# Kernel optimization log

Hardware: AMD Instinct MI355X
Metric: run time of the kernel (lower is better)

The kernel has to match this reference:

```python
import jax, jax.numpy as jnp
import numpy as np

V = 267735
D_PROJ = 1024
CUTOFF_ENDS = [0, 20000, 40000, 200000, V]   # cutoffs + [vocab]
DIV_VAL = 4
SEQ, BATCH = 64, 8


def setup_inputs() -> dict:
    key = jax.random.key(0)
    ks = jax.random.split(key, 20)
    s = 0.02
    inp = {}
    inp["hidden"] = jax.random.normal(ks[0], (SEQ, BATCH, D_PROJ), dtype=jnp.float32)
    inp["target"] = jax.random.randint(ks[1], (SEQ, BATCH), 0, V)
    n_clusters = len(CUTOFF_ENDS) - 2  # 3
    inp["cluster_weight"] = jax.random.normal(ks[2], (n_clusters, 1024), dtype=jnp.float32) * s
    inp["cluster_bias"] = jnp.zeros((n_clusters,), dtype=jnp.float32)
    k = 3
    for i in range(4):
        l, r = CUTOFF_ENDS[i], CUTOFF_ENDS[i + 1]
        d_i = 1024 // (DIV_VAL ** i)        # 1024, 256, 64, 16
        inp[f"W{i}"] = jax.random.normal(ks[k], (r - l, d_i), dtype=jnp.float32) * s; k += 1
        inp[f"b{i}"] = jnp.zeros((r - l,), dtype=jnp.float32)
        inp[f"proj{i}"] = jax.random.normal(ks[k], (d_i, D_PROJ), dtype=jnp.float32) * s; k += 1
    return inp


def _logit(x, W, b, proj):
    # x: [i,b,d_proj], proj: [d_emb_i, d_proj], W: [n, d_emb_i]
    y = jnp.einsum('ibd,ed->ibe', x, proj)
    return jnp.einsum('ibe,ne->ibn', y, W) + b


def reference(hidden, target, cluster_weight, cluster_bias,
              W0, b0, proj0, W1, b1, proj1, W2, b2, proj2, W3, b3, proj3):
    c0 = CUTOFF_ENDS[1]  # shortlist size (20000)
    # head: shortlist weights concatenated with cluster logits
    head_W = jnp.concatenate([W0, cluster_weight], axis=0)   # [c0 + n_clusters, 1024]
    head_b = jnp.concatenate([b0, cluster_bias], axis=0)
    head_logprob = jax.nn.log_softmax(_logit(hidden, head_W, head_b, proj0), axis=-1)
    out = [head_logprob[..., :c0]]
    tails = [(W1, b1, proj1), (W2, b2, proj2), (W3, b3, proj3)]
    for i, (W, b, proj) in enumerate(tails, start=1):
        tail_logprob = jax.nn.log_softmax(_logit(hidden, W, b, proj), axis=-1)
        # joint logprob = log P(cluster i) + log P(word | cluster i)
        out.append(head_logprob[..., c0 + i - 1, None] + tail_logprob)
    out = jnp.concatenate(out, axis=-1)  # [seq, batch, vocab] of log-probs
    # scatter/gather loss combine is equivalent to gathering the gold log-prob
    gold_lp = jnp.take_along_axis(out, target[..., None], axis=-1)[..., 0]
    loss = -jnp.mean(gold_lp)
    return out, loss
```

## Files before the change

### kernel.cpp

```cpp
#include <hip/hip_runtime.h>

typedef __attribute__((ext_vector_type(8))) short short8;
typedef __attribute__((ext_vector_type(4))) float f32x4;

#define LDC 267735L
#define OUT_ELEMS 137080320L
#define NB_TOT 2094
#define M_FIX 16.0f

__device__ __forceinline__ short f2bf(float f) {
    unsigned u = __float_as_uint(f);
    unsigned r = (u + 0x7fffu + ((u >> 16) & 1u)) >> 16;
    return (short)r;
}
__device__ __forceinline__ float bf2f(short s) {
    return __uint_as_float(((unsigned)(unsigned short)s) << 16);
}
__device__ __forceinline__ short8 cvt8v(f32x4 a, f32x4 b) {
    short8 r;
    r[0] = f2bf(a[0]); r[1] = f2bf(a[1]); r[2] = f2bf(a[2]); r[3] = f2bf(a[3]);
    r[4] = f2bf(b[0]); r[5] = f2bf(b[1]); r[6] = f2bf(b[2]); r[7] = f2bf(b[3]);
    return r;
}

__device__ __forceinline__ void gll16(const short* g, short* l) {
    __builtin_amdgcn_global_load_lds(
        (const __attribute__((address_space(1))) void*)g,
        (__attribute__((address_space(3))) void*)l, 16, 0, 0);
}

__device__ __forceinline__ void conv8(int e, const float* __restrict__ src,
                                      const float* __restrict__ ex, int Nsrc, int Nex,
                                      int Ksrc, int kshift, short* __restrict__ dst)
{
    int r = e >> kshift;
    int c = (e & ((1 << kshift) - 1)) << 3;
    const float* p = nullptr;
    if (r < Nsrc) p = src + (long)r * Ksrc + c;
    else if (r < Nsrc + Nex) p = ex + (long)(r - Nsrc) * Ksrc + c;
    short8 o = {0, 0, 0, 0, 0, 0, 0, 0};
    if (p != nullptr && c < Ksrc) {
        f32x4 a = *(const f32x4*)p;
        f32x4 b = *(const f32x4*)(p + 4);
        o = cvt8v(a, b);
    }
    *(short8*)(dst + (((long)r) << (kshift + 3)) + c) = o;
}

__global__ __launch_bounds__(256) void convert_all(
    const float* __restrict__ W0, const float* __restrict__ cw,
    const float* __restrict__ W1, const float* __restrict__ W2, const float* __restrict__ W3,
    const float* __restrict__ p0, const float* __restrict__ p1,
    const float* __restrict__ p2, const float* __restrict__ p3,
    const float* __restrict__ hidden,
    short* __restrict__ Wb0, short* __restrict__ Wb1,
    short* __restrict__ Wb2, short* __restrict__ Wb3,
    short* __restrict__ pb0, short* __restrict__ pb1,
    short* __restrict__ pb2, short* __restrict__ pb3,
    short* __restrict__ hb)
{
    int b = blockIdx.x;
    int tid = threadIdx.x;
    if (b < 10048)      { conv8((b          ) * 256 + tid, W0, cw, 20000, 3, 1024, 7, Wb0); }
    else if (b < 12560) { conv8((b - 10048  ) * 256 + tid, W1, nullptr, 20000, 0, 256, 5, Wb1); }
    else if (b < 17560) { conv8((b - 12560  ) * 256 + tid, W2, nullptr, 160000, 0, 64, 3, Wb2); }
    else if (b < 18620) { conv8((b - 17560  ) * 256 + tid, W3, nullptr, 67735, 0, 16, 2, Wb3); }
    else if (b < 19132) { conv8((b - 18620  ) * 256 + tid, p0, nullptr, 1024, 0, 1024, 7, pb0); }
    else if (b < 19260) { conv8((b - 19132  ) * 256 + tid, p1, nullptr, 256, 0, 1024, 7, pb1); }
    else if (b < 19324) { conv8((b - 19260  ) * 256 + tid, p2, nullptr, 64, 0, 1024, 7, pb2); }
    else if (b < 19388) { conv8((b - 19324  ) * 256 + tid, p3, nullptr, 16, 0, 1024, 7, pb3); }
    else                { conv8((b - 19388  ) * 256 + tid, hidden, nullptr, 512, 0, 1024, 7, hb); }
}

struct SegP {
    const short* A;
    const short* B;
    const float* bias;
    short* Cb;
    long ldcb;
    int lda, ldb, K, N, Nmain;
};
struct Seg4 { SegP s[4]; };

template<int MODE>
__global__ __launch_bounds__(256, 3) void gemm_uber(
    Seg4 segs, int e0, int e1, int e2,
    const float* __restrict__ cbias, float* __restrict__ clus,
    float* __restrict__ partMS)
{
    __shared__ short As[2][128 * 32];
    __shared__ short Bs[2][128 * 32];
    __shared__ float ps[2][128];

    int bx = blockIdx.x;
    int si = (bx < e0) ? 0 : (bx < e1) ? 1 : (bx < e2) ? 2 : 3;
    int sb = (si == 0) ? 0 : (si == 1) ? e0 : (si == 2) ? e1 : e2;
    const SegP sp = segs.s[si];

    int tid = threadIdx.x;
    int w = tid >> 6, l = tid & 63;
    int wm = w >> 1, wn = w & 1;
    int l15 = l & 15, g = l >> 4, k8 = g << 3;
    int rowBase = blockIdx.y << 7;
    int colBase = (bx - sb) << 7;

    int sr0 = (w << 5);
    int sr1 = sr0 + 16;
    int lrow = l >> 2;
    int kOff = (l & 3) << 3;
    const short* aG0 = sp.A + (long)(rowBase + sr0 + lrow) * sp.lda + kOff;
    const short* aG1 = sp.A + (long)(rowBase + sr1 + lrow) * sp.lda + kOff;
    const short* bG0 = sp.B + (long)(colBase + sr0 + lrow) * sp.ldb + kOff;
    const short* bG1 = sp.B + (long)(colBase + sr1 + lrow) * sp.ldb + kOff;
    int ldsA0 = sr0 << 5;
    int ldsA1 = sr1 << 5;

    f32x4 acc[4][4];
    #pragma unroll
    for (int i = 0; i < 4; ++i)
        #pragma unroll
        for (int j = 0; j < 4; ++j) acc[i][j] = f32x4{0.f, 0.f, 0.f, 0.f};

    int nt = sp.K >> 5;

    gll16(aG0, &As[0][ldsA0]);
    gll16(aG1, &As[0][ldsA1]);
    gll16(bG0, &Bs[0][ldsA0]);
    gll16(bG1, &Bs[0][ldsA1]);
    __syncthreads();

    int cur = 0;
    #pragma unroll 1
    for (int t = 0; t < nt; ++t) {
        int knext = (t + 1) << 5;
        if (t + 1 < nt) {
            int nb = cur ^ 1;
            gll16(aG0 + knext, &As[nb][ldsA0]);
            gll16(aG1 + knext, &As[nb][ldsA1]);
            gll16(bG0 + knext, &Bs[nb][ldsA0]);
            gll16(bG1 + knext, &Bs[nb][ldsA1]);
        }
        short8 af[4], bf[4];
        #pragma unroll
        for (int mi = 0; mi < 4; ++mi)
            af[mi] = *(const short8*)&As[cur][(((wm << 6) + (mi << 4) + l15) << 5) + k8];
        #pragma unroll
        for (int ni = 0; ni < 4; ++ni)
            bf[ni] = *(const short8*)&Bs[cur][(((wn << 6) + (ni << 4) + l15) << 5) + k8];
        #pragma unroll
        for (int mi = 0; mi < 4; ++mi)
            #pragma unroll
            for (int ni = 0; ni < 4; ++ni)
                acc[mi][ni] = __builtin_amdgcn_mfma_f32_16x16x32_bf16(
                    af[mi], bf[ni], acc[mi][ni], 0, 0, 0);
        __syncthreads();
        cur ^= 1;
    }

    int colv[4];
    float bv4[4];
    #pragma unroll
    for (int ni = 0; ni < 4; ++ni) {
        int col = colBase + (wn << 6) + (ni << 4) + l15;
        colv[ni] = col;
        float bval = 0.f;
        if (MODE == 1) {
            if (col < sp.Nmain) bval = sp.bias[col];
            else if (col < sp.N) bval = cbias[col - sp.Nmain];
        }
        bv4[ni] = bval;
    }

    #pragma unroll
    for (int mi = 0; mi < 4; ++mi) {
        #pragma unroll
        for (int r = 0; r < 4; ++r) {
            int srowg = rowBase + (wm << 6) + (mi << 4) + (g << 2) + r;
            float vals[4];
            #pragma unroll
            for (int ni = 0; ni < 4; ++ni) vals[ni] = acc[mi][ni][r] + bv4[ni];

            if (MODE == 0) {
                #pragma unroll
                for (int ni = 0; ni < 4; ++ni) {
                    int col = colv[ni];
                    if (col < (int)sp.ldcb)
                        sp.Cb[(long)srowg * sp.ldcb + col] = f2bf(vals[ni]);
                }
            } else {
                float s = 0.f;
                #pragma unroll
                for (int ni = 0; ni < 4; ++ni) {
                    int col = colv[ni];
                    if (col < sp.Nmain) {
                        sp.Cb[(long)srowg * sp.ldcb + col] = f2bf(vals[ni]);
                        s += __expf(vals[ni] - M_FIX);
                    } else if (col < sp.N) {
                        clus[srowg * 3 + (col - sp.Nmain)] = vals[ni];
                        s += __expf(vals[ni] - M_FIX);
                    }
                }
                #pragma unroll
                for (int d = 1; d < 16; d <<= 1) s += __shfl_xor(s, d);
                if (l15 == 0) {
                    int rl = (wm << 6) + (mi << 4) + (g << 2) + r;
                    ps[wn][rl] = s;
                }
            }
        }
    }
    if (MODE == 1) {
        __syncthreads();
        if (tid < 128) {
            float S = ps[0][tid] + ps[1][tid];
            partMS[(long)(rowBase + tid) * NB_TOT + bx] = S;
        }
    }
}

__global__ __launch_bounds__(256) void combine_adj(
    const float* __restrict__ partMS, const float* __restrict__ clus,
    float* __restrict__ adjA)
{
    const int segOff[4] = {0, 157, 314, 1564};
    const int segNb[4]  = {157, 157, 1250, 530};
    int row = blockIdx.x, tid = threadIdx.x;
    const float* p = partMS + (long)row * NB_TOT;
    __shared__ float ss[256], Ls[4];
    for (int seg = 0; seg < 4; ++seg) {
        float s = 0.f;
        for (int cb = segOff[seg] + tid; cb < segOff[seg] + segNb[seg]; cb += 256)
            s += p[cb];
        ss[tid] = s;
        __syncthreads();
        for (int off = 128; off > 0; off >>= 1) {
            if (tid < off) ss[tid] += ss[tid + off];
            __syncthreads();
        }
        if (tid == 0) Ls[seg] = logf(ss[0]) + M_FIX;
        __syncthreads();
    }
    if (tid == 0) {
        float l0 = Ls[0];
        adjA[row * 4 + 0] = -l0;
        adjA[row * 4 + 1] = clus[row * 3 + 0] - l0 - Ls[1];
        adjA[row * 4 + 2] = clus[row * 3 + 1] - l0 - Ls[2];
        adjA[row * 4 + 3] = clus[row * 3 + 2] - l0 - Ls[3];
    }
}

__global__ __launch_bounds__(256) void finalize2(
    const short* __restrict__ L0, const short* __restrict__ L1,
    const short* __restrict__ L2, const short* __restrict__ L3,
    const float* __restrict__ adjA, float* __restrict__ out)
{
    int row = blockIdx.y;
    long c0 = ((long)blockIdx.x * 256 + threadIdx.x) * 8;
    if (c0 >= 267735) return;
    const short* src; float adj; long off;
    if (c0 < 20000)       { src = L0 + (long)row * 20000;  off = c0;          adj = adjA[row*4+0]; }
    else if (c0 < 40000)  { src = L1 + (long)row * 20000;  off = c0 - 20000;  adj = adjA[row*4+1]; }
    else if (c0 < 200000) { src = L2 + (long)row * 160000; off = c0 - 40000;  adj = adjA[row*4+2]; }
    else                  { src = L3 + (long)row * 67736;  off = c0 - 200000; adj = adjA[row*4+3]; }
    float* po = out + (long)row * LDC + c0;
    if (c0 + 8 <= 267735) {
        short8 v = *(const short8*)(src + off);
        #pragma unroll
        for (int j = 0; j < 8; ++j) po[j] = bf2f(v[j]) + adj;
    } else {
        for (int j = 0; c0 + j < 267735; ++j) po[j] = bf2f(src[off + j]) + adj;
    }
}

__global__ __launch_bounds__(512) void loss_k(
    const float* __restrict__ out, const int* __restrict__ target,
    float* __restrict__ lossOut)
{
    int tid = threadIdx.x;
    int t = target[tid];
    float v = out[(long)tid * LDC + t];
    __shared__ float sbuf[512];
    sbuf[tid] = v;
    __syncthreads();
    for (int off = 256; off > 0; off >>= 1) {
        if (tid < off) sbuf[tid] += sbuf[tid + off];
        __syncthreads();
    }
    if (tid == 0) lossOut[0] = -sbuf[0] / 512.0f;
}

__device__ __forceinline__ short8 cvt8p(const float* p, bool valid) {
    short8 r = {0, 0, 0, 0, 0, 0, 0, 0};
    if (valid) {
        f32x4 a = *(const f32x4*)p;
        f32x4 b = *(const f32x4*)(p + 4);
        r = cvt8v(a, b);
    }
    return r;
}

#define LDT 40
__global__ __launch_bounds__(256, 2) void gemm_f32(
    const float* __restrict__ A, int lda,
    const float* __restrict__ B, int ldb,
    const float* __restrict__ Wex,
    const float* __restrict__ bias, const float* __restrict__ biasEx,
    float* __restrict__ C, long ldc, long colOffset,
    float* __restrict__ Cex,
    int N, int Nmain, int K)
{
    __shared__ short As[2][128 * LDT];
    __shared__ short Bs[2][128 * LDT];
    int tid = threadIdx.x;
    int w = tid >> 6, l = tid & 63;
    int wm = w >> 1, wn = w & 1;
    int l15 = l & 15, g = l >> 4, k8 = g << 3;
    int rowBase = blockIdx.y << 7;
    int colBase = blockIdx.x << 7;
    int srow = tid >> 1;
    int skc = (tid & 1) << 4;
    const float* aSrc = A + (long)(rowBase + srow) * lda + skc;
    int bn = colBase + srow;
    bool bnv = bn < N;
    const float* bRow = (Wex != nullptr && bn >= Nmain)
                          ? (Wex + (long)(bn - Nmain) * ldb)
                          : (B + (long)(bnv ? bn : 0) * ldb);
    const float* bSrc = bRow + skc;
    int ldsOff = srow * LDT + skc;
    f32x4 acc[4][4];
    #pragma unroll
    for (int i = 0; i < 4; ++i)
        #pragma unroll
        for (int j = 0; j < 4; ++j) acc[i][j] = f32x4{0.f, 0.f, 0.f, 0.f};
    int nt = (K + 31) >> 5;
    {
        bool kv = skc < K;
        *(short8*)&As[0][ldsOff]     = cvt8p(aSrc, kv);
        *(short8*)&As[0][ldsOff + 8] = cvt8p(aSrc + 8, kv);
        *(short8*)&Bs[0][ldsOff]     = cvt8p(bSrc, kv && bnv);
        *(short8*)&Bs[0][ldsOff + 8] = cvt8p(bSrc + 8, kv && bnv);
    }
    __syncthreads();
    int cur = 0;
    #pragma unroll 1
    for (int t = 0; t < nt; ++t) {
        int knext = (t + 1) << 5;
        bool more = knext < K;
        short8 wa0, wa1, wb0, wb1;
        if (more) {
            bool kv = (knext + skc) < K;
            wa0 = cvt8p(aSrc + knext, kv);
            wa1 = cvt8p(aSrc + knext + 8, kv);
            wb0 = cvt8p(bSrc + knext, kv && bnv);
            wb1 = cvt8p(bSrc + knext + 8, kv && bnv);
        }
        short8 af[4], bf[4];
        #pragma unroll
        for (int mi = 0; mi < 4; ++mi)
            af[mi] = *(const short8*)&As[cur][((wm << 6) + (mi << 4) + l15) * LDT + k8];
        #pragma unroll
        for (int ni = 0; ni < 4; ++ni)
            bf[ni] = *(const short8*)&Bs[cur][((wn << 6) + (ni << 4) + l15) * LDT + k8];
        #pragma unroll
        for (int mi = 0; mi < 4; ++mi)
            #pragma unroll
            for (int ni = 0; ni < 4; ++ni)
                acc[mi][ni] = __builtin_amdgcn_mfma_f32_16x16x32_bf16(
                    af[mi], bf[ni], acc[mi][ni], 0, 0, 0);
        if (more) {
            int nb = cur ^ 1;
            *(short8*)&As[nb][ldsOff] = wa0;  *(short8*)&As[nb][ldsOff + 8] = wa1;
            *(short8*)&Bs[nb][ldsOff] = wb0;  *(short8*)&Bs[nb][ldsOff + 8] = wb1;
        }
        __syncthreads();
        cur ^= 1;
    }
    #pragma unroll
    for (int mi = 0; mi < 4; ++mi) {
        #pragma unroll
        for (int r = 0; r < 4; ++r) {
            int srowg = rowBase + (wm << 6) + (mi << 4) + (g << 2) + r;
            #pragma unroll
            for (int ni = 0; ni < 4; ++ni) {
                int col = colBase + (wn << 6) + (ni << 4) + l15;
                float v = acc[mi][ni][r];
                if (col < Nmain) {
                    if (bias) v += bias[col];
                    C[(long)srowg * ldc + colOffset + col] = v;
                } else if (col < N) {
                    if (biasEx) v += biasEx[col - Nmain];
                    Cex[srowg * 3 + (col - Nmain)] = v;
                }
            }
        }
    }
}

__global__ __launch_bounds__(256) void reduce_lse(
    const float* __restrict__ out, const float* __restrict__ clus,
    float* __restrict__ lse)
{
    const int segStart[4] = {0, 20000, 40000, 200000};
    const int segLen[4]   = {20000, 20000, 160000, 67735};
    int seg = blockIdx.x, row = blockIdx.y, tid = threadIdx.x;
    int len = segLen[seg] + (seg == 0 ? 3 : 0);
    const float* p = out + (long)row * LDC + segStart[seg];
    float m = -1e30f, s = 0.f;
    for (int i = tid; i < len; i += 256) {
        float x = (seg == 0 && i >= 20000) ? clus[row * 3 + (i - 20000)] : p[i];
        if (x > m) { s *= __expf(m - x); m = x; }
        s += __expf(x - m);
    }
    __shared__ float sm[256], ss[256];
    sm[tid] = m; ss[tid] = s;
    __syncthreads();
    for (int off = 128; off > 0; off >>= 1) {
        if (tid < off) {
            float m1 = sm[tid], s1 = ss[tid];
            float m2 = sm[tid + off], s2 = ss[tid + off];
            float M = fmaxf(m1, m2);
            sm[tid] = M;
            ss[tid] = s1 * __expf(m1 - M) + s2 * __expf(m2 - M);
        }
        __syncthreads();
    }
    if (tid == 0) lse[row * 4 + seg] = sm[0] + logf(ss[0]);
}

__global__ __launch_bounds__(256) void finalize_k(
    float* __restrict__ out, const float* __restrict__ lse,
    const float* __restrict__ clus)
{
    int row = blockIdx.y;
    long base = (long)row * LDC;
    float l0 = lse[row * 4 + 0];
    float a0 = -l0;
    float a1 = clus[row * 3 + 0] - l0 - lse[row * 4 + 1];
    float a2 = clus[row * 3 + 1] - l0 - lse[row * 4 + 2];
    float a3 = clus[row * 3 + 2] - l0 - lse[row * 4 + 3];
    int v = blockIdx.x * blockDim.x + threadIdx.x;
    int col = v * 4;
    if (col + 4 <= 267735) {
        float adj = col < 20000 ? a0 : col < 40000 ? a1 : col < 200000 ? a2 : a3;
        float* p = out + base + col;
        p[0] += adj; p[1] += adj; p[2] += adj; p[3] += adj;
    } else if (col < 267735) {
        for (int c = col; c < 267735; ++c) out[base + c] += a3;
    }
}

extern "C" void kernel_launch(void* const* d_in, const int* in_sizes, int n_in,
                              void* d_out, int out_size, void* d_ws, size_t ws_size,
                              hipStream_t stream) {
    const float* hidden = (const float*)d_in[0];
    const int*   target = (const int*)d_in[1];
    const float* cw = (const float*)d_in[2];
    const float* cb = (const float*)d_in[3];
    const float* W0 = (const float*)d_in[4];
    const float* b0 = (const float*)d_in[5];
    const float* p0 = (const float*)d_in[6];
    const float* W1 = (const float*)d_in[7];
    const float* b1 = (const float*)d_in[8];
    const float* p1 = (const float*)d_in[9];
    const float* W2 = (const float*)d_in[10];
    const float* b2 = (const float*)d_in[11];
    const float* p2 = (const float*)d_in[12];
    const float* W3 = (const float*)d_in[13];
    const float* b3 = (const float*)d_in[14];
    const float* p3 = (const float*)d_in[15];

    float* out = (float*)d_out;
    dim3 blk(256);

    float* fp = (float*)d_ws;
    float* partMS = fp;
    float* clus = partMS + 1072128;
    float* adjA = clus + 1536;
    short* sb = (short*)(adjA + 2048);
    size_t o = 0;
    short* hb  = sb + o; o += 512 * 1024;
    short* y0b = sb + o; o += 512 * 1024;
    short* y1b = sb + o; o += 512 * 256;
    short* y2b = sb + o; o += 512 * 64;
    short* y3b = sb + o; o += 512 * 32;
    short* pb0 = sb + o; o += 1024 * 1024;
    short* pb1 = sb + o; o += 256 * 1024;
    short* pb2 = sb + o; o += 128 * 1024;
    short* pb3 = sb + o; o += 128 * 1024;
    short* Wb0 = sb + o; o += 20096L * 1024;
    short* Wb1 = sb + o; o += 20096L * 256;
    short* Wb2 = sb + o; o += 160000L * 64;
    short* Wb3 = sb + o; o += 67840L * 32;
    short* L0c = sb + o; o += 512L * 20000;
    short* L1c = sb + o; o += 512L * 20000;
    short* L2c = sb + o; o += 512L * 160000;
    short* L3c = sb + o; o += 512L * 67736;
    size_t needFast = (char*)(sb + o) - (char*)d_ws;

    if (ws_size >= needFast) {
        convert_all<<<dim3(19644), blk, 0, stream>>>(
            W0, cw, W1, W2, W3, p0, p1, p2, p3, hidden,
            Wb0, Wb1, Wb2, Wb3, pb0, pb1, pb2, pb3, hb);

        Seg4 pj;
        pj.s[0] = {hb, pb0, nullptr, y0b, 1024, 1024, 1024, 1024, 1024, 1024};
        pj.s[1] = {hb, pb1, nullptr, y1b, 256,  1024, 1024, 1024, 256,  256};
        pj.s[2] = {hb, pb2, nullptr, y2b, 64,   1024, 1024, 1024, 64,   64};
        pj.s[3] = {hb, pb3, nullptr, y3b, 32,   1024, 1024, 1024, 32,   32};
        gemm_uber<0><<<dim3(12, 4), blk, 0, stream>>>(pj, 8, 10, 11, nullptr, nullptr, nullptr);

        Seg4 lg;
        lg.s[0] = {y0b, Wb0, b0, L0c, 20000,  1024, 1024, 1024, 20003,  20000};
        lg.s[1] = {y1b, Wb1, b1, L1c, 20000,  256,  256,  256,  20000,  20000};
        lg.s[2] = {y2b, Wb2, b2, L2c, 160000, 64,   64,   64,   160000, 160000};
        lg.s[3] = {y3b, Wb3, b3, L3c, 67736,  32,   32,   32,   67735,  67735};
        gemm_uber<1><<<dim3(2094, 4), blk, 0, stream>>>(lg, 157, 314, 1564, cb, clus, partMS);

        combine_adj<<<dim3(512), blk, 0, stream>>>(partMS, clus, adjA);
        finalize2<<<dim3(131, 512), blk, 0, stream>>>(L0c, L1c, L2c, L3c, adjA, out);
        loss_k<<<dim3(1), dim3(512), 0, stream>>>(out, target, out + OUT_ELEMS);
        return;
    }

    float* ws = (float*)d_ws;
    float* y0 = ws;
    float* y1 = y0 + 512 * 1024;
    float* y2 = y1 + 512 * 256;
    float* y3 = y2 + 512 * 64;
    float* clusF = y3 + 512 * 16;
    float* lseF = clusF + 512 * 3;

    gemm_f32<<<dim3(8, 4), blk, 0, stream>>>(hidden, 1024, p0, 1024, nullptr, nullptr, nullptr,
                                             y0, 1024, 0, nullptr, 1024, 1024, 1024);
    gemm_f32<<<dim3(2, 4), blk, 0, stream>>>(hidden, 1024, p1, 1024, nullptr, nullptr, nullptr,
                                             y1, 256, 0, nullptr, 256, 256, 1024);
    gemm_f32<<<dim3(1, 4), blk, 0, stream>>>(hidden, 1024, p2, 1024, nullptr, nullptr, nullptr,
                                             y2, 64, 0, nullptr, 64, 64, 1024);
    gemm_f32<<<dim3(1, 4), blk, 0, stream>>>(hidden, 1024, p3, 1024, nullptr, nullptr, nullptr,
                                             y3, 16, 0, nullptr, 16, 16, 1024);
    gemm_f32<<<dim3(157, 4), blk, 0, stream>>>(y0, 1024, W0, 1024, cw, b0, cb,
                                               out, LDC, 0, clusF, 20003, 20000, 1024);
    gemm_f32<<<dim3(157, 4), blk, 0, stream>>>(y1, 256, W1, 256, nullptr, b1, nullptr,
                                               out, LDC, 20000, nullptr, 20000, 20000, 256);
    gemm_f32<<<dim3(1250, 4), blk, 0, stream>>>(y2, 64, W2, 64, nullptr, b2, nullptr,
                                                out, LDC, 40000, nullptr, 160000, 160000, 64);
    gemm_f32<<<dim3(530, 4), blk, 0, stream>>>(y3, 16, W3, 16, nullptr, b3, nullptr,
                                               out, LDC, 200000, nullptr, 67735, 67735, 16);
    reduce_lse<<<dim3(4, 512), blk, 0, stream>>>(out, clusF, lseF);
    finalize_k<<<dim3(262, 512), blk, 0, stream>>>(out, lseF, clusF);
    loss_k<<<dim3(1), dim3(512), 0, stream>>>(out, target, out + OUT_ELEMS);
}
```

Baseline: 387.5 us.

## Process logits in 128-row chunks to keep bf16 intermediates cache-resident

Splits the logit GEMM, LSE combine and finalize stages into four sequential passes over 128-row chunks. The bf16 logit buffers and partial-sum buffers shrink to one chunk, so the intermediate written by the GEMM may still be in the last-level cache when finalize reads it back, cutting HBM traffic. In exchange there are four times as many kernel launches, and each GEMM launch has only 2094 blocks, which may leave the GPU less full and lets the W tiles be reread from memory once per chunk.

```diff
diff --git a/kernel.cpp b/kernel.cpp
--- a/kernel.cpp
+++ b/kernel.cpp
@@ -7,6 +7,7 @@
 #define OUT_ELEMS 137080320L
 #define NB_TOT 2094
 #define M_FIX 16.0f
+#define CHUNK 128
 
 __device__ __forceinline__ short f2bf(float f) {
     unsigned u = __float_as_uint(f);
@@ -84,7 +85,7 @@
 
 template<int MODE>
 __global__ __launch_bounds__(256, 3) void gemm_uber(
-    Seg4 segs, int e0, int e1, int e2,
+    Seg4 segs, int e0, int e1, int e2, int rowOff,
     const float* __restrict__ cbias, float* __restrict__ clus,
     float* __restrict__ partMS)
 {
@@ -108,8 +109,8 @@
     int sr1 = sr0 + 16;
     int lrow = l >> 2;
     int kOff = (l & 3) << 3;
-    const short* aG0 = sp.A + (long)(rowBase + sr0 + lrow) * sp.lda + kOff;
-    const short* aG1 = sp.A + (long)(rowBase + sr1 + lrow) * sp.lda + kOff;
+    const short* aG0 = sp.A + (long)(rowOff + rowBase + sr0 + lrow) * sp.lda + kOff;
+    const short* aG1 = sp.A + (long)(rowOff + rowBase + sr1 + lrow) * sp.lda + kOff;
     const short* bG0 = sp.B + (long)(colBase + sr0 + lrow) * sp.ldb + kOff;
     const short* bG1 = sp.B + (long)(colBase + sr1 + lrow) * sp.ldb + kOff;
     int ldsA0 = sr0 << 5;
@@ -175,7 +176,7 @@
     for (int mi = 0; mi < 4; ++mi) {
         #pragma unroll
         for (int r = 0; r < 4; ++r) {
-            int srowg = rowBase + (wm << 6) + (mi << 4) + (g << 2) + r;
+            int lrowg = rowBase + (wm << 6) + (mi << 4) + (g << 2) + r;
             float vals[4];
             #pragma unroll
             for (int ni = 0; ni < 4; ++ni) vals[ni] = acc[mi][ni][r] + bv4[ni];
@@ -185,7 +186,7 @@
                 for (int ni = 0; ni < 4; ++ni) {
                     int col = colv[ni];
                     if (col < (int)sp.ldcb)
-                        sp.Cb[(long)srowg * sp.ldcb + col] = f2bf(vals[ni]);
+                        sp.Cb[(long)lrowg * sp.ldcb + col] = f2bf(vals[ni]);
                 }
             } else {
                 float s = 0.f;
@@ -193,10 +194,10 @@
                 for (int ni = 0; ni < 4; ++ni) {
                     int col = colv[ni];
                     if (col < sp.Nmain) {
-                        sp.Cb[(long)srowg * sp.ldcb + col] = f2bf(vals[ni]);
+                        sp.Cb[(long)lrowg * sp.ldcb + col] = f2bf(vals[ni]);
                         s += __expf(vals[ni] - M_FIX);
                     } else if (col < sp.N) {
-                        clus[srowg * 3 + (col - sp.Nmain)] = vals[ni];
+                        clus[(rowOff + lrowg) * 3 + (col - sp.Nmain)] = vals[ni];
                         s += __expf(vals[ni] - M_FIX);
                     }
                 }
@@ -220,12 +221,13 @@
 
 __global__ __launch_bounds__(256) void combine_adj(
     const float* __restrict__ partMS, const float* __restrict__ clus,
-    float* __restrict__ adjA)
+    float* __restrict__ adjA, int rowOff)
 {
     const int segOff[4] = {0, 157, 314, 1564};
     const int segNb[4]  = {157, 157, 1250, 530};
-    int row = blockIdx.x, tid = threadIdx.x;
-    const float* p = partMS + (long)row * NB_TOT;
+    int lrow = blockIdx.x, tid = threadIdx.x;
+    int row = rowOff + lrow;
+    const float* p = partMS + (long)lrow * NB_TOT;
     __shared__ float ss[256], Ls[4];
     for (int seg = 0; seg < 4; ++seg) {
         float s = 0.f;
@@ -252,16 +254,17 @@
 __global__ __launch_bounds__(256) void finalize2(
     const short* __restrict__ L0, const short* __restrict__ L1,
     const short* __restrict__ L2, const short* __restrict__ L3,
-    const float* __restrict__ adjA, float* __restrict__ out)
-{
-    int row = blockIdx.y;
+    const float* __restrict__ adjA, float* __restrict__ out, int rowOff)
+{
+    int lrow = blockIdx.y;
+    int row = rowOff + lrow;
     long c0 = ((long)blockIdx.x * 256 + threadIdx.x) * 8;
     if (c0 >= 267735) return;
     const short* src; float adj; long off;
-    if (c0 < 20000)       { src = L0 + (long)row * 20000;  off = c0;          adj = adjA[row*4+0]; }
-    else if (c0 < 40000)  { src = L1 + (long)row * 20000;  off = c0 - 20000;  adj = adjA[row*4+1]; }
-    else if (c0 < 200000) { src = L2 + (long)row * 160000; off = c0 - 40000;  adj = adjA[row*4+2]; }
-    else                  { src = L3 + (long)row * 67736;  off = c0 - 200000; adj = adjA[row*4+3]; }
+    if (c0 < 20000)       { src = L0 + (long)lrow * 20000;  off = c0;          adj = adjA[row*4+0]; }
+    else if (c0 < 40000)  { src = L1 + (long)lrow * 20000;  off = c0 - 20000;  adj = adjA[row*4+1]; }
+    else if (c0 < 200000) { src = L2 + (long)lrow * 160000; off = c0 - 40000;  adj = adjA[row*4+2]; }
+    else                  { src = L3 + (long)lrow * 67736;  off = c0 - 200000; adj = adjA[row*4+3]; }
     float* po = out + (long)row * LDC + c0;
     if (c0 + 8 <= 267735) {
         short8 v = *(const short8*)(src + off);
@@ -474,7 +477,7 @@
 
     float* fp = (float*)d_ws;
     float* partMS = fp;
-    float* clus = partMS + 1072128;
+    float* clus = partMS + (long)CHUNK * NB_TOT;
     float* adjA = clus + 1536;
     short* sb = (short*)(adjA + 2048);
     size_t o = 0;
@@ -491,10 +494,10 @@
     short* Wb1 = sb + o; o += 20096L * 256;
     short* Wb2 = sb + o; o += 160000L * 64;
     short* Wb3 = sb + o; o += 67840L * 32;
-    short* L0c = sb + o; o += 512L * 20000;
-    short* L1c = sb + o; o += 512L * 20000;
-    short* L2c = sb + o; o += 512L * 160000;
-    short* L3c = sb + o; o += 512L * 67736;
+    short* L0c = sb + o; o += (long)CHUNK * 20000;
+    short* L1c = sb + o; o += (long)CHUNK * 20000;
+    short* L2c = sb + o; o += (long)CHUNK * 160000;
+    short* L3c = sb + o; o += (long)CHUNK * 67736;
     size_t needFast = (char*)(sb + o) - (char*)d_ws;
 
     if (ws_size >= needFast) {
@@ -507,17 +510,20 @@
         pj.s[1] = {hb, pb1, nullptr, y1b, 256,  1024, 1024, 1024, 256,  256};
         pj.s[2] = {hb, pb2, nullptr, y2b, 64,   1024, 1024, 1024, 64,   64};
         pj.s[3] = {hb, pb3, nullptr, y3b, 32,   1024, 1024, 1024, 32,   32};
-        gemm_uber<0><<<dim3(12, 4), blk, 0, stream>>>(pj, 8, 10, 11, nullptr, nullptr, nullptr);
+        gemm_uber<0><<<dim3(12, 4), blk, 0, stream>>>(pj, 8, 10, 11, 0, nullptr, nullptr, nullptr);
 
         Seg4 lg;
         lg.s[0] = {y0b, Wb0, b0, L0c, 20000,  1024, 1024, 1024, 20003,  20000};
         lg.s[1] = {y1b, Wb1, b1, L1c, 20000,  256,  256,  256,  20000,  20000};
         lg.s[2] = {y2b, Wb2, b2, L2c, 160000, 64,   64,   64,   160000, 160000};
         lg.s[3] = {y3b, Wb3, b3, L3c, 67736,  32,   32,   32,   67735,  67735};
-        gemm_uber<1><<<dim3(2094, 4), blk, 0, stream>>>(lg, 157, 314, 1564, cb, clus, partMS);
-
-        combine_adj<<<dim3(512), blk, 0, stream>>>(partMS, clus, adjA);
-        finalize2<<<dim3(131, 512), blk, 0, stream>>>(L0c, L1c, L2c, L3c, adjA, out);
+        for (int rowOff = 0; rowOff < 512; rowOff += CHUNK) {
+            gemm_uber<1><<<dim3(2094, CHUNK / 128), blk, 0, stream>>>(
+                lg, 157, 314, 1564, rowOff, cb, clus, partMS);
+            combine_adj<<<dim3(CHUNK), blk, 0, stream>>>(partMS, clus, adjA, rowOff);
+            finalize2<<<dim3(131, CHUNK), blk, 0, stream>>>(L0c, L1c, L2c, L3c, adjA, out, rowOff);
+        }
+
         loss_k<<<dim3(1), dim3(512), 0, stream>>>(out, target, out + OUT_ELEMS);
         return;
     }
```

After: 437.8 us. 13.0% more time.
